# Performance work log

Measured on AMD Instinct MI355X. Metric: run time of the kernel, lower is better.

Reference implementation:

```python
import jax, jax.numpy as jnp
import numpy as np

TLAMBDA = 0.5
DELTA = 0.1
PROP_LAYERS = 2
LN_EPS = 1e-12
MASK_NEG = -10000.0
N_HEADS = 4


def _ln(x, g, b):
    m = x.mean(-1, keepdims=True)
    v = ((x - m) ** 2).mean(-1, keepdims=True)
    return (x - m) * jax.lax.rsqrt(v + LN_EPS) * g + b


def _l2norm(x):
    # F.normalize(p=2, dim=-1) with eps=1e-12
    n = jnp.sqrt((x * x).sum(-1, keepdims=True))
    return x / jnp.maximum(n, 1e-12)


def _sparse_prop(op):
    # op: [B, N, 2] rows of (col_idx, weight). result[b,j,m] = w_j*w_m if idx_j==idx_m else 0
    idx = op[..., 0].astype(jnp.int32)
    w = op[..., 1]
    eq = idx[:, :, None] == idx[:, None, :]
    return jnp.where(eq, w[:, :, None] * w[:, None, :], jnp.zeros((), op.dtype))


def _prop(t, P):
    enc = t
    for _ in range(PROP_LAYERS):
        t = jnp.einsum('bnm,bme->bne', P, t) + DELTA * enc
    return t


def _bert_layer(h, mask, Wq, bq, Wk, bk, Wv, bv, Wo, bo, g1, b1, Wi, bi, Wf, bf, g2, b2):
    AN, S, E = h.shape
    dh = E // N_HEADS

    def heads(x):
        return x.reshape(AN, S, N_HEADS, dh).transpose(0, 2, 1, 3)

    q = heads(h @ Wq + bq)
    k = heads(h @ Wk + bk)
    v = heads(h @ Wv + bv)
    scores = jnp.einsum('ahsd,ahtd->ahst', q, k) / np.float32(np.sqrt(dh)) + mask
    probs = jax.nn.softmax(scores, axis=-1)
    ctx = jnp.einsum('ahst,ahtd->ahsd', probs, v).transpose(0, 2, 1, 3).reshape(AN, S, E)
    a = _ln(ctx @ Wo + bo + h, g1, b1)
    f = jax.nn.gelu(a @ Wi + bi, approximate=False)
    return _ln(f @ Wf + bf + a, g2, b2)


def reference(token_edges_batch, hidden_states, attention_mask, query_embedding, key_embedding,
              user_operator, item_operator, distance_embedding, centrality_embedding,
              Wq, bq, Wk, bk, Wv, bv, Wo, bo, ln_att_g, ln_att_b, Wi, bi, Wf, bf, ln_ffn_g, ln_ffn_b,
              W_agg, b_agg, W_d1, b_d1, ln1_g, ln1_b, W_d2, b_d2, ln2_g, ln2_b):
    B, N, _ = token_edges_batch.shape
    AN, S, E = hidden_states.shape
    L = Wq.shape[0]

    U = _sparse_prop(user_operator)   # [B, N, N]
    I = _sparse_prop(item_operator)
    sub_next_q = jnp.zeros((B, N, E), hidden_states.dtype)
    sub_next_k = jnp.zeros((B, N, E), hidden_states.dtype)
    mask0 = attention_mask.at[..., :4].set(MASK_NEG)

    hs = hidden_states.reshape(B, N, S, E)
    all_hs = []
    for i in range(L):
        all_hs.append(hs)
        if i > 0:
            hs = (hs.at[:, :, 0].set(query_embedding)
                    .at[:, :, 1].set(key_embedding)
                    .at[:, :, 2].set(distance_embedding)
                    .at[:, :, 3].set(centrality_embedding))
        p1 = _ln(_prop(TLAMBDA * query_embedding + sub_next_q, U) @ W_d1 + b_d1, ln1_g, ln1_b)
        p2 = _ln(_prop(TLAMBDA * key_embedding + sub_next_k, I) @ W_d2 + b_d2, ln2_g, ln2_b)
        mask = mask0 if i == 0 else attention_mask
        h = _bert_layer(hs.reshape(AN, S, E), mask,
                        Wq[i], bq[i], Wk[i], bk[i], Wv[i], bv[i], Wo[i], bo[i],
                        ln_att_g[i], ln_att_b[i], Wi[i], bi[i], Wf[i], bf[i], ln_ffn_g[i], ln_ffn_b[i])
        hs = h.reshape(B, N, S, E)
        sub_next_q = hs[:, :, 0, :]
        sub_next_k = hs[:, :, 1, :]
        snt = _l2norm(hs[:, 0, 4, :])                       # [B, E]
        p = jnp.concatenate([snt, p1[:, 0, :], p2[:, 1, :]], axis=1)  # [B, 3E]
        agg = _l2norm(jax.nn.relu(p @ W_agg[i] + b_agg[i]))
        hs = hs.at[:, 0, 4, :].set(agg)
    all_hs.append(hs)

    out1 = all_hs[L - 1][:, 0, 4:, :].mean(axis=1)
    out2 = all_hs[L][:, 0, 4:, :].mean(axis=1)
    return 0.5 * (out1 + out2)


def setup_inputs() -> dict:
    key = jax.random.key(0)
    ks = jax.random.split(key, 40)
    B, N, S, E, L, FF = 64, 64, 32, 256, 2, 1024
    AN = B * N
    f = jnp.float32
    inp = {}
    inp['token_edges_batch'] = jax.random.randint(ks[0], (B, N, 8), 0, 100)
    inp['hidden_states'] = jax.random.normal(ks[1], (AN, S, E), f)
    inp['attention_mask'] = jnp.zeros((AN, 1, 1, S), f)
    inp['query_embedding'] = jax.random.normal(ks[2], (B, N, E), f)
    inp['key_embedding'] = jax.random.normal(ks[3], (B, N, E), f)
    inp['distance_embedding'] = jax.random.normal(ks[4], (B, N, E), f)
    inp['centrality_embedding'] = jax.random.normal(ks[5], (B, N, E), f)

    def make_op(k1, k2):
        idx = jax.random.randint(k1, (B, N), 0, 16).astype(f)
        w = jax.random.uniform(k2, (B, N), f)
        return jnp.stack([idx, w], axis=-1)

    inp['user_operator'] = make_op(ks[6], ks[7])
    inp['item_operator'] = make_op(ks[8], ks[9])

    sc = 0.02
    def w(k, shape):
        return jax.random.normal(k, shape, f) * sc

    inp['Wq'] = w(ks[10], (L, E, E)); inp['bq'] = jnp.zeros((L, E), f)
    inp['Wk'] = w(ks[11], (L, E, E)); inp['bk'] = jnp.zeros((L, E), f)
    inp['Wv'] = w(ks[12], (L, E, E)); inp['bv'] = jnp.zeros((L, E), f)
    inp['Wo'] = w(ks[13], (L, E, E)); inp['bo'] = jnp.zeros((L, E), f)
    inp['ln_att_g'] = jnp.ones((L, E), f); inp['ln_att_b'] = jnp.zeros((L, E), f)
    inp['Wi'] = w(ks[14], (L, E, FF)); inp['bi'] = jnp.zeros((L, FF), f)
    inp['Wf'] = w(ks[15], (L, FF, E)); inp['bf'] = jnp.zeros((L, E), f)
    inp['ln_ffn_g'] = jnp.ones((L, E), f); inp['ln_ffn_b'] = jnp.zeros((L, E), f)
    inp['W_agg'] = w(ks[16], (L, 3 * E, E)); inp['b_agg'] = jnp.zeros((L, E), f)
    inp['W_d1'] = w(ks[17], (E, E)); inp['b_d1'] = jnp.zeros((E,), f)
    inp['ln1_g'] = jnp.ones((E,), f); inp['ln1_b'] = jnp.zeros((E,), f)
    inp['W_d2'] = w(ks[18], (E, E)); inp['b_d2'] = jnp.zeros((E,), f)
    inp['ln2_g'] = jnp.ones((E,), f); inp['ln2_b'] = jnp.zeros((E,), f)
    return inp
```

## Files before the change

kernel.cpp:

```cpp
#include <hip/hip_runtime.h>
#include <math.h>

#define E 256
#define SEQ 32
#define FF 1024
#define NEG_MASK -10000.0f

typedef __attribute__((ext_vector_type(8))) short bf16x8;
typedef __attribute__((ext_vector_type(4))) short s16x4;
typedef __attribute__((ext_vector_type(4))) float f32x4;
typedef __attribute__((ext_vector_type(16))) float f32x16;

__device__ __forceinline__ float bf2f(unsigned short u) {
  unsigned v = ((unsigned)u) << 16; float f; __builtin_memcpy(&f, &v, 4); return f;
}
__device__ __forceinline__ unsigned short f2bf(float f) {
  unsigned u; __builtin_memcpy(&u, &f, 4);
  unsigned r = (u + 0x7fffu + ((u >> 16) & 1u)) >> 16;
  return (unsigned short)r;
}
__device__ __forceinline__ s16x4 f2bf4(float4 v) {
  s16x4 r;
  r[0] = (short)f2bf(v.x); r[1] = (short)f2bf(v.y);
  r[2] = (short)f2bf(v.z); r[3] = (short)f2bf(v.w);
  return r;
}
__device__ __forceinline__ f32x4 mfma16(bf16x8 a, bf16x8 b, f32x4 c) {
  return __builtin_amdgcn_mfma_f32_16x16x32_bf16(a, b, c, 0, 0, 0);
}
__device__ __forceinline__ f32x16 mfma32(bf16x8 a, bf16x8 b, f32x16 c) {
  return __builtin_amdgcn_mfma_f32_32x32x16_bf16(a, b, c, 0, 0, 0);
}
__device__ __forceinline__ float block_sum256(float v, float* tmp4) {
  #pragma unroll
  for (int o = 32; o > 0; o >>= 1) v += __shfl_down(v, o);
  int wid = threadIdx.x >> 6, lane = threadIdx.x & 63;
  if (lane == 0) tmp4[wid] = v;
  __syncthreads();
  float r = tmp4[0] + tmp4[1] + tmp4[2] + tmp4[3];
  __syncthreads();
  return r;
}

__global__ __launch_bounds__(256) void wprep_kernel(
    const float* __restrict__ Wq, const float* __restrict__ Wk,
    const float* __restrict__ Wv, const float* __restrict__ Wo,
    const float* __restrict__ Wi, const float* __restrict__ Wf,
    unsigned short* wqt, unsigned short* wkt, unsigned short* wvt,
    unsigned short* wot, unsigned short* wit, unsigned short* wft) {
  int type = blockIdx.y, ll = blockIdx.z, t = threadIdx.x;
  const float* src; unsigned short* dst; int Kd, Nd, m32;
  switch (type) {
    case 0: src = Wq + (size_t)ll * 65536;  dst = wqt + (size_t)ll * 65536;  Kd = 256;  Nd = 256;  m32 = 0; break;
    case 1: src = Wk + (size_t)ll * 65536;  dst = wkt + (size_t)ll * 65536;  Kd = 256;  Nd = 256;  m32 = 0; break;
    case 2: src = Wv + (size_t)ll * 65536;  dst = wvt + (size_t)ll * 65536;  Kd = 256;  Nd = 256;  m32 = 0; break;
    case 3: src = Wo + (size_t)ll * 65536;  dst = wot + (size_t)ll * 65536;  Kd = 256;  Nd = 256;  m32 = 0; break;
    case 4: src = Wi + (size_t)ll * 262144; dst = wit + (size_t)ll * 262144; Kd = 256;  Nd = 1024; m32 = 1; break;
    default: src = Wf + (size_t)ll * 262144; dst = wft + (size_t)ll * 262144; Kd = 1024; Nd = 256; m32 = 1; break;
  }
  int frag = blockIdx.x * 4 + (t >> 6);
  int l = t & 63;
  int nkc = m32 ? (Kd >> 4) : (Kd >> 5);
  int nfrag = (m32 ? (Nd >> 5) : (Nd >> 4)) * nkc;
  if (frag >= nfrag) return;
  int n, k0;
  if (m32) { n = (frag / nkc) * 32 + (l & 31); k0 = (frag % nkc) * 16 + (l >> 5) * 8; }
  else     { n = (frag / nkc) * 16 + (l & 15); k0 = (frag % nkc) * 32 + (l >> 4) * 8; }
  unsigned short vv[8];
  #pragma unroll
  for (int j = 0; j < 8; ++j) vv[j] = f2bf(src[(size_t)(k0 + j) * Nd + n]);
  unsigned short* o = dst + (size_t)frag * 512 + l * 8;
  #pragma unroll
  for (int j = 0; j < 8; ++j) o[j] = vv[j];
}

__global__ __launch_bounds__(256) void prop_ln_kernel(
    const float* __restrict__ emb_q, const float* __restrict__ emb_k,
    const float* snq,
    const float* __restrict__ uop, const float* __restrict__ iop,
    const float* __restrict__ Wd1, const float* __restrict__ bd1,
    const float* __restrict__ g1v, const float* __restrict__ b1v,
    const float* __restrict__ Wd2, const float* __restrict__ bd2,
    const float* __restrict__ g2v, const float* __restrict__ b2v,
    float* __restrict__ out1, float* __restrict__ out2) {
  int sel = blockIdx.y;
  const float* emb = sel ? emb_k : emb_q;
  const float* op  = sel ? iop : uop;
  const float* Wd  = sel ? Wd2 : Wd1;
  const float* bd  = sel ? bd2 : bd1;
  const float* g   = sel ? g2v : g1v;
  const float* bvec= sel ? b2v : b1v;
  float* outp      = sel ? out2 : out1;
  int row = sel;
  __shared__ float s1[16 * E];
  __shared__ float s2[16 * E];
  __shared__ float wv[64];
  __shared__ int gi[64];
  __shared__ float t2row[E];
  __shared__ float tmp4[4];
  int b = blockIdx.x, e = threadIdx.x;
  if (e < 64) {
    wv[e] = op[(b * 64 + e) * 2 + 1];
    gi[e] = (int)op[(b * 64 + e) * 2 + 0];
  }
  for (int gg = 0; gg < 16; ++gg) { s1[gg * E + e] = 0.f; s2[gg * E + e] = 0.f; }
  __syncthreads();
  float t0r = 0.f;
  for (int n = 0; n < 64; ++n) {
    float t0 = 0.5f * emb[(size_t)(b * 64 + n) * E + e];
    if (snq) t0 += snq[((size_t)(b * 64 + n) * 2 + sel) * E + e];
    if (n == row) t0r = t0;
    s1[gi[n] * E + e] += wv[n] * t0;
  }
  for (int n = 0; n < 64; ++n) {
    float t0 = 0.5f * emb[(size_t)(b * 64 + n) * E + e];
    if (snq) t0 += snq[((size_t)(b * 64 + n) * 2 + sel) * E + e];
    float t1 = wv[n] * s1[gi[n] * E + e] + 0.1f * t0;
    s2[gi[n] * E + e] += wv[n] * t1;
  }
  float t2 = wv[row] * s2[gi[row] * E + e] + 0.1f * t0r;
  t2row[e] = t2;
  __syncthreads();
  float y = bd[e];
  for (int k = 0; k < E; ++k) y = fmaf(t2row[k], Wd[k * E + e], y);
  float ssum = block_sum256(y, tmp4);
  float qsum = block_sum256(y * y, tmp4);
  float m = ssum * (1.f / E);
  float var = qsum * (1.f / E) - m * m;
  outp[b * E + e] = (y - m) * rsqrtf(var + 1e-12f) * g[e] + bvec[e];
}

__global__ __launch_bounds__(256, 4) void seq_attn_mfma(
    const float* __restrict__ hidden,
    const unsigned short* __restrict__ wqt, const float* __restrict__ bq,
    const unsigned short* __restrict__ wkt, const float* __restrict__ bk,
    const unsigned short* __restrict__ wvt, const float* __restrict__ bv,
    const float* __restrict__ mask, unsigned short* __restrict__ ctx_all,
    unsigned short* __restrict__ Kf, unsigned short* __restrict__ Vf) {
  __shared__ __align__(16) unsigned short aT[32][264];
  __shared__ __align__(16) unsigned short kvb[32][272];
  __shared__ __align__(16) unsigned short qs16[2][264];
  __shared__ float pr[4][2][36];
  int a = blockIdx.x, t = threadIdx.x;
  int w = t >> 6, l = t & 63;
  int lm = l & 15, lkq = l >> 4, lk = lkq << 3;
  size_t hb = (size_t)a * (SEQ * E);
  #pragma unroll
  for (int i = 0; i < 8; ++i) {
    int p = i * 256 + t; int row = p >> 6, c4 = (p & 63) << 2;
    float4 v = *(const float4*)&hidden[hb + row * E + c4];
    *(s16x4*)&aT[row][c4] = f2bf4(v);
  }
  __syncthreads();
  bool isn0 = ((a & 63) == 0);
  int nb = a >> 6;
  f32x4 zz = {0.f, 0.f, 0.f, 0.f};
  #pragma unroll
  for (int nt = 0; nt < 4; ++nt) {
    int ncol = w * 64 + nt * 16 + lm;
    const unsigned short* bkrow = wkt + ((size_t)(w * 4 + nt) * 8) * 512 + l * 8;
    const unsigned short* bqrow = wqt + ((size_t)(w * 4 + nt) * 8) * 512 + l * 8;
    bf16x8 bk8[8], bq8[8];
    #pragma unroll
    for (int kc = 0; kc < 8; ++kc) bk8[kc] = *(const bf16x8*)(bkrow + kc * 512);
    #pragma unroll
    for (int kc = 0; kc < 8; ++kc) bq8[kc] = *(const bf16x8*)(bqrow + kc * 512);
    f32x4 ak0 = zz, ak1 = zz, aq = zz;
    #pragma unroll
    for (int kc = 0; kc < 8; ++kc) {
      bf16x8 a0 = *(const bf16x8*)&aT[lm][kc * 32 + lk];
      bf16x8 a1 = *(const bf16x8*)&aT[16 + lm][kc * 32 + lk];
      ak0 = mfma16(a0, bk8[kc], ak0);
      ak1 = mfma16(a1, bk8[kc], ak1);
      aq  = mfma16(a0, bq8[kc], aq);
    }
    float bb = bk[ncol];
    #pragma unroll
    for (int r = 0; r < 4; ++r) {
      int rw = (lkq << 2) + r;
      float v0 = ak0[r] + bb, v1 = ak1[r] + bb;
      kvb[rw][ncol] = f2bf(v0);
      kvb[16 + rw][ncol] = f2bf(v1);
      if (isn0) {
        Kf[((size_t)nb * 32 + rw) * 256 + ncol] = f2bf(v0);
        Kf[((size_t)nb * 32 + 16 + rw) * 256 + ncol] = f2bf(v1);
      }
    }
    if (lkq == 0) {
      float bqv = bq[ncol];
      qs16[0][ncol] = f2bf(aq[0] + bqv);
      qs16[1][ncol] = f2bf(aq[1] + bqv);
    }
  }
  __syncthreads();
  {
    f32x4 sc0 = zz, sc1 = zz;
    #pragma unroll
    for (int kc2 = 0; kc2 < 2; ++kc2) {
      bf16x8 aq = *(const bf16x8*)&qs16[lm & 1][w * 64 + kc2 * 32 + lk];
      bf16x8 b0 = *(const bf16x8*)&kvb[lm][w * 64 + kc2 * 32 + lk];
      bf16x8 b1 = *(const bf16x8*)&kvb[16 + lm][w * 64 + kc2 * 32 + lk];
      sc0 = mfma16(aq, b0, sc0);
      sc1 = mfma16(aq, b1, sc1);
    }
    float mv0 = (lm < 4) ? NEG_MASK : mask[(size_t)a * SEQ + lm];
    float mv1 = mask[(size_t)a * SEQ + 16 + lm];
    #pragma unroll
    for (int r = 0; r < 2; ++r) {
      float s0 = sc0[r] * 0.125f + mv0;
      float s1 = sc1[r] * 0.125f + mv1;
      float mx = fmaxf(s0, s1);
      mx = fmaxf(mx, __shfl_xor(mx, 1));
      mx = fmaxf(mx, __shfl_xor(mx, 2));
      mx = fmaxf(mx, __shfl_xor(mx, 4));
      mx = fmaxf(mx, __shfl_xor(mx, 8));
      float e0 = expf(s0 - mx), e1 = expf(s1 - mx);
      float se = e0 + e1;
      se += __shfl_xor(se, 1); se += __shfl_xor(se, 2);
      se += __shfl_xor(se, 4); se += __shfl_xor(se, 8);
      float inv = 1.f / se;
      if (lkq == 0) {
        pr[w][r][lm] = e0 * inv;
        pr[w][r][16 + lm] = e1 * inv;
      }
    }
  }
  __syncthreads();
  #pragma unroll
  for (int nt = 0; nt < 4; ++nt) {
    int ncol = w * 64 + nt * 16 + lm;
    const unsigned short* bvrow = wvt + ((size_t)(w * 4 + nt) * 8) * 512 + l * 8;
    bf16x8 bv8[8];
    #pragma unroll
    for (int kc = 0; kc < 8; ++kc) bv8[kc] = *(const bf16x8*)(bvrow + kc * 512);
    f32x4 av0 = zz, av1 = zz;
    #pragma unroll
    for (int kc = 0; kc < 8; ++kc) {
      bf16x8 a0 = *(const bf16x8*)&aT[lm][kc * 32 + lk];
      bf16x8 a1 = *(const bf16x8*)&aT[16 + lm][kc * 32 + lk];
      av0 = mfma16(a0, bv8[kc], av0);
      av1 = mfma16(a1, bv8[kc], av1);
    }
    float bb = bv[ncol];
    #pragma unroll
    for (int r = 0; r < 4; ++r) {
      int rw = (lkq << 2) + r;
      float v0 = av0[r] + bb, v1 = av1[r] + bb;
      kvb[rw][ncol] = f2bf(v0);
      kvb[16 + rw][ncol] = f2bf(v1);
      if (isn0) {
        Vf[((size_t)nb * 32 + rw) * 256 + ncol] = f2bf(v0);
        Vf[((size_t)nb * 32 + 16 + rw) * 256 + ncol] = f2bf(v1);
      }
    }
  }
  __syncthreads();
  {
    float o0 = 0.f, o1 = 0.f;
    #pragma unroll
    for (int tt = 0; tt < 32; ++tt) {
      float vv = bf2f(kvb[tt][t]);
      o0 = fmaf(pr[w][0][tt], vv, o0);
      o1 = fmaf(pr[w][1][tt], vv, o1);
    }
    ctx_all[((size_t)a * 2 + 0) * E + t] = f2bf(o0);
    ctx_all[((size_t)a * 2 + 1) * E + t] = f2bf(o1);
  }
}

__global__ __launch_bounds__(256) void gemm_bias_kernel(
    const float* __restrict__ Af, const unsigned short* __restrict__ Bt,
    const float* __restrict__ bias, unsigned short* __restrict__ outb) {
  __shared__ __align__(16) unsigned short aT[32][264];
  int t = threadIdx.x, w = t >> 6, l = t & 63;
  int lm = l & 15, lkq = l >> 4, lk = lkq << 3;
  int row0 = blockIdx.x * 32;
  #pragma unroll
  for (int i = 0; i < 8; ++i) {
    int p = i * 256 + t; int row = p >> 6, c4 = (p & 63) << 2;
    int gr = row0 + row;
    int src = ((gr >> 5) << 11) + (gr & 31);
    float4 v = *(const float4*)&Af[(size_t)src * E + c4];
    *(s16x4*)&aT[row][c4] = f2bf4(v);
  }
  __syncthreads();
  f32x4 zz = {0.f, 0.f, 0.f, 0.f};
  #pragma unroll
  for (int nt = 0; nt < 4; ++nt) {
    int ncol = w * 64 + nt * 16 + lm;
    const unsigned short* brow = Bt + ((size_t)(w * 4 + nt) * 8) * 512 + l * 8;
    bf16x8 b8[8];
    #pragma unroll
    for (int kc = 0; kc < 8; ++kc) b8[kc] = *(const bf16x8*)(brow + kc * 512);
    f32x4 c0 = zz, c1 = zz;
    #pragma unroll
    for (int kc = 0; kc < 8; ++kc) {
      bf16x8 a0 = *(const bf16x8*)&aT[lm][kc * 32 + lk];
      bf16x8 a1 = *(const bf16x8*)&aT[16 + lm][kc * 32 + lk];
      c0 = mfma16(a0, b8[kc], c0);
      c1 = mfma16(a1, b8[kc], c1);
    }
    float bb = bias[ncol];
    #pragma unroll
    for (int r = 0; r < 4; ++r) {
      int rw = (lkq << 2) + r;
      outb[(size_t)(row0 + rw) * E + ncol] = f2bf(c0[r] + bb);
      outb[(size_t)(row0 + 16 + rw) * E + ncol] = f2bf(c1[r] + bb);
    }
  }
}

__global__ __launch_bounds__(256) void qkv1_kernel(
    const unsigned short* __restrict__ Ab,
    const unsigned short* __restrict__ wq, const float* __restrict__ bqv,
    const unsigned short* __restrict__ wk, const float* __restrict__ bkv,
    const unsigned short* __restrict__ wv, const float* __restrict__ bvv,
    unsigned short* q2, unsigned short* k2, unsigned short* v2) {
  __shared__ __align__(16) unsigned short aT[32][264];
  int t = threadIdx.x, w = t >> 6, l = t & 63;
  int lm = l & 15, lkq = l >> 4, lk = lkq << 3;
  int row0 = blockIdx.x * 32;
  int m = blockIdx.y;
  const unsigned short* Wt = (m == 0) ? wq : (m == 1) ? wk : wv;
  const float* bb = (m == 0) ? bqv : (m == 1) ? bkv : bvv;
  unsigned short* outb = (m == 0) ? q2 : (m == 1) ? k2 : v2;
  #pragma unroll
  for (int i = 0; i < 4; ++i) {
    int p = i * 256 + t; int row = p >> 5, c8 = (p & 31) << 3;
    *(s16x4*)&aT[row][c8] = *(const s16x4*)&Ab[(size_t)(row0 + row) * E + c8];
    *(s16x4*)&aT[row][c8 + 4] = *(const s16x4*)&Ab[(size_t)(row0 + row) * E + c8 + 4];
  }
  __syncthreads();
  f32x4 zz = {0.f, 0.f, 0.f, 0.f};
  #pragma unroll
  for (int nt = 0; nt < 4; ++nt) {
    int ncol = w * 64 + nt * 16 + lm;
    const unsigned short* brow = Wt + ((size_t)(w * 4 + nt) * 8) * 512 + l * 8;
    bf16x8 b8[8];
    #pragma unroll
    for (int kc = 0; kc < 8; ++kc) b8[kc] = *(const bf16x8*)(brow + kc * 512);
    f32x4 c0 = zz, c1 = zz;
    #pragma unroll
    for (int kc = 0; kc < 8; ++kc) {
      bf16x8 a0 = *(const bf16x8*)&aT[lm][kc * 32 + lk];
      bf16x8 a1 = *(const bf16x8*)&aT[16 + lm][kc * 32 + lk];
      c0 = mfma16(a0, b8[kc], c0);
      c1 = mfma16(a1, b8[kc], c1);
    }
    float bv2 = bb[ncol];
    #pragma unroll
    for (int r = 0; r < 4; ++r) {
      int rw = (lkq << 2) + r;
      outb[(size_t)(row0 + rw) * E + ncol] = f2bf(c0[r] + bv2);
      outb[(size_t)(row0 + 16 + rw) * E + ncol] = f2bf(c1[r] + bv2);
    }
  }
}

__global__ __launch_bounds__(256) void attnf_kernel(
    const unsigned short* __restrict__ Q, const unsigned short* __restrict__ K,
    const unsigned short* __restrict__ V, unsigned short* __restrict__ CTX,
    const float* __restrict__ mask, int set4) {
  int b = blockIdx.x, h = blockIdx.y, t = threadIdx.x;
  __shared__ float qsh[32][65], ksh[32][65], vsh[32][65];
  __shared__ float pr[32][33];
  size_t base = (size_t)b * (SEQ * E) + h * 64;
  for (int i = 0; i < 8; ++i) {
    int p = i * 256 + t; int s = p >> 6, d = p & 63;
    qsh[s][d] = bf2f(Q[base + s * E + d]);
    ksh[s][d] = bf2f(K[base + s * E + d]);
    vsh[s][d] = bf2f(V[base + s * E + d]);
  }
  __syncthreads();
  for (int i = 0; i < 4; ++i) {
    int p = i * 256 + t; int s = p >> 5, tt = p & 31;
    float acc = 0.f;
    #pragma unroll
    for (int d = 0; d < 64; ++d) acc = fmaf(qsh[s][d], ksh[tt][d], acc);
    float mv = mask[(size_t)b * 2048 + tt];
    if (set4 && tt < 4) mv = NEG_MASK;
    pr[s][tt] = acc * 0.125f + mv;
  }
  __syncthreads();
  int rrow = t >> 3, l8 = t & 7;
  float vals[4];
  float mx = -1e30f;
  #pragma unroll
  for (int ii = 0; ii < 4; ++ii) { vals[ii] = pr[rrow][l8 + ii * 8]; mx = fmaxf(mx, vals[ii]); }
  mx = fmaxf(mx, __shfl_xor(mx, 1));
  mx = fmaxf(mx, __shfl_xor(mx, 2));
  mx = fmaxf(mx, __shfl_xor(mx, 4));
  float se = 0.f;
  #pragma unroll
  for (int ii = 0; ii < 4; ++ii) { vals[ii] = expf(vals[ii] - mx); se += vals[ii]; }
  se += __shfl_xor(se, 1); se += __shfl_xor(se, 2); se += __shfl_xor(se, 4);
  float inv = 1.f / se;
  #pragma unroll
  for (int ii = 0; ii < 4; ++ii) pr[rrow][l8 + ii * 8] = vals[ii] * inv;
  __syncthreads();
  for (int i = 0; i < 8; ++i) {
    int p = i * 256 + t; int s = p >> 6, d = p & 63;
    float acc = 0.f;
    #pragma unroll
    for (int tt = 0; tt < SEQ; ++tt) acc = fmaf(pr[s][tt], vsh[tt][d], acc);
    CTX[base + s * E + d] = f2bf(acc);
  }
}

__device__ __forceinline__ int map_res(int gr) {
  if (gr < 8192) return ((gr >> 1) << 5) + (gr & 1);
  int rr = gr - 8192;
  return ((rr >> 5) << 11) + (rr & 31);
}

__global__ __launch_bounds__(256) void tailA_mfma(
    const unsigned short* __restrict__ ctx,
    const unsigned short* __restrict__ wo, const float* __restrict__ bo,
    const float* __restrict__ Res, int resmode,
    const float* __restrict__ g1, const float* __restrict__ b1,
    unsigned short* __restrict__ a_bf, float* __restrict__ a_f32) {
  __shared__ __align__(16) unsigned short aT[32][264];
  __shared__ float sT[32][257];
  __shared__ float prs[32][4], prq[32][4];
  int t = threadIdx.x, w = t >> 6, l = t & 63;
  int row0 = blockIdx.x * 32;
  #pragma unroll
  for (int i = 0; i < 8; ++i) {
    int p = i * 256 + t; int row = p >> 6, c4 = (p & 63) << 2;
    *(s16x4*)&aT[row][c4] = *(const s16x4*)&ctx[(size_t)(row0 + row) * E + c4];
  }
  __syncthreads();
  {
    int lm = l & 15, lkq = l >> 4, lk = lkq << 3;
    f32x4 zz = {0.f, 0.f, 0.f, 0.f};
    #pragma unroll
    for (int nt = 0; nt < 4; ++nt) {
      int ncol = w * 64 + nt * 16 + lm;
      const unsigned short* brow = wo + ((size_t)(w * 4 + nt) * 8) * 512 + l * 8;
      bf16x8 b8[8];
      #pragma unroll
      for (int kc = 0; kc < 8; ++kc) b8[kc] = *(const bf16x8*)(brow + kc * 512);
      f32x4 c0 = zz, c1 = zz;
      #pragma unroll
      for (int kc = 0; kc < 8; ++kc) {
        bf16x8 a0 = *(const bf16x8*)&aT[lm][kc * 32 + lk];
        bf16x8 a1 = *(const bf16x8*)&aT[16 + lm][kc * 32 + lk];
        c0 = mfma16(a0, b8[kc], c0);
        c1 = mfma16(a1, b8[kc], c1);
      }
      float bb = bo[ncol];
      #pragma unroll
      for (int r = 0; r < 4; ++r) {
        int rw = (lkq << 2) + r;
        int rr0 = resmode ? map_res(row0 + rw) : (row0 + rw);
        int rr1 = resmode ? map_res(row0 + 16 + rw) : (row0 + 16 + rw);
        sT[rw][ncol] = c0[r] + bb + Res[(size_t)rr0 * E + ncol];
        sT[16 + rw][ncol] = c1[r] + bb + Res[(size_t)rr1 * E + ncol];
      }
    }
  }
  __syncthreads();
  {
    int wid = t >> 6, lane = t & 63;
    float vcache[32];
    for (int r = 0; r < 32; ++r) {
      float v = sT[r][t];
      vcache[r] = v;
      float s = v, q = v * v;
      #pragma unroll
      for (int o = 32; o > 0; o >>= 1) { s += __shfl_down(s, o); q += __shfl_down(q, o); }
      if (lane == 0) { prs[r][wid] = s; prq[r][wid] = q; }
    }
    __syncthreads();
    #pragma unroll
    for (int r = 0; r < 32; ++r) {
      float Sv = prs[r][0] + prs[r][1] + prs[r][2] + prs[r][3];
      float Qv = prq[r][0] + prq[r][1] + prq[r][2] + prq[r][3];
      float m = Sv * (1.f / E), var = Qv * (1.f / E) - m * m;
      float val = (vcache[r] - m) * rsqrtf(var + 1e-12f) * g1[t] + b1[t];
      a_f32[(size_t)(row0 + r) * E + t] = val;
      a_bf[(size_t)(row0 + r) * E + t] = f2bf(val);
    }
  }
}

__global__ __launch_bounds__(512) void ffnB_kernel(
    const unsigned short* __restrict__ a_bf,
    const unsigned short* __restrict__ wi, const float* __restrict__ bi,
    const unsigned short* __restrict__ wf,
    unsigned short* __restrict__ part, size_t pstride) {
  __shared__ __align__(16) unsigned short aT[32][264];
  __shared__ __align__(16) unsigned short fT[32][264];
  int t = threadIdx.x, w = t >> 6, l = t & 63;
  int lm = l & 31, lk = (l >> 5) << 3;
  int row0 = blockIdx.x * 32, qh = blockIdx.y;
  #pragma unroll
  for (int i = 0; i < 2; ++i) {
    int chunk = i * 512 + t; int row = chunk >> 5, c8 = (chunk & 31) << 3;
    *(s16x4*)&aT[row][c8] = *(const s16x4*)&a_bf[(size_t)(row0 + row) * E + c8];
    *(s16x4*)&aT[row][c8 + 4] = *(const s16x4*)&a_bf[(size_t)(row0 + row) * E + c8 + 4];
  }
  __syncthreads();
  f32x16 zz16 = {0};
  {
    const unsigned short* brow = wi + ((size_t)(qh * 8 + w) * 16) * 512 + l * 8;
    bf16x8 b16[16];
    #pragma unroll
    for (int kc = 0; kc < 16; ++kc) b16[kc] = *(const bf16x8*)(brow + kc * 512);
    f32x16 c = zz16;
    #pragma unroll
    for (int kc = 0; kc < 16; ++kc) {
      bf16x8 a = *(const bf16x8*)&aT[lm][kc * 16 + lk];
      c = mfma32(a, b16[kc], c);
    }
    int lcol = w * 32 + lm;
    float bib = bi[qh * 256 + lcol];
    #pragma unroll
    for (int reg = 0; reg < 16; ++reg) {
      int row = (reg & 3) + 8 * (reg >> 2) + 4 * (l >> 5);
      float x = c[reg] + bib;
      fT[row][lcol] = f2bf(0.5f * x * (1.f + erff(x * 0.70710678118654752f)));
    }
  }
  __syncthreads();
  {
    const unsigned short* brow = wf + ((size_t)(w * 64 + qh * 16)) * 512 + l * 8;
    bf16x8 b16[16];
    #pragma unroll
    for (int kc = 0; kc < 16; ++kc) b16[kc] = *(const bf16x8*)(brow + kc * 512);
    f32x16 c = zz16;
    #pragma unroll
    for (int kc = 0; kc < 16; ++kc) {
      bf16x8 a = *(const bf16x8*)&fT[lm][kc * 16 + lk];
      c = mfma32(a, b16[kc], c);
    }
    unsigned short* po = part + (size_t)qh * pstride;
    int col = w * 32 + lm;
    #pragma unroll
    for (int reg = 0; reg < 16; ++reg) {
      int row = (reg & 3) + 8 * (reg >> 2) + 4 * (l >> 5);
      po[(size_t)(row0 + row) * E + col] = f2bf(c[reg]);
    }
  }
}

__global__ __launch_bounds__(256) void ffnC_kernel(
    const unsigned short* __restrict__ part, size_t pstride,
    const float* __restrict__ bfv, const float* __restrict__ a_f32,
    const float* __restrict__ g2, const float* __restrict__ b2,
    float* __restrict__ out0, float* __restrict__ out1, int split) {
  __shared__ float prs[32][4], prq[32][4];
  int t = threadIdx.x;
  int row0 = blockIdx.x * 32;
  int wid = t >> 6, lane = t & 63;
  float bb = bfv[t];
  float vcache[32];
  for (int r = 0; r < 32; ++r) {
    size_t idx = (size_t)(row0 + r) * E + t;
    float v = bf2f(part[idx]) + bf2f(part[pstride + idx]) +
              bf2f(part[2 * pstride + idx]) + bf2f(part[3 * pstride + idx]) +
              bb + a_f32[idx];
    vcache[r] = v;
    float s = v, q = v * v;
    #pragma unroll
    for (int o = 32; o > 0; o >>= 1) { s += __shfl_down(s, o); q += __shfl_down(q, o); }
    if (lane == 0) { prs[r][wid] = s; prq[r][wid] = q; }
  }
  __syncthreads();
  #pragma unroll
  for (int r = 0; r < 32; ++r) {
    float Sv = prs[r][0] + prs[r][1] + prs[r][2] + prs[r][3];
    float Qv = prq[r][0] + prq[r][1] + prq[r][2] + prq[r][3];
    float m = Sv * (1.f / E), var = Qv * (1.f / E) - m * m;
    float val = (vcache[r] - m) * rsqrtf(var + 1e-12f) * g2[t] + b2[t];
    int gr = row0 + r;
    if (gr < split) out0[(size_t)gr * E + t] = val;
    else            out1[(size_t)(gr - split) * E + t] = val;
  }
}

__global__ __launch_bounds__(256) void agg_build_kernel(
    const float* __restrict__ h1n0,
    const float* __restrict__ p1, const float* __restrict__ p2,
    const float* __restrict__ Wagg, const float* __restrict__ bagg,
    const float* __restrict__ qe, const float* __restrict__ ke,
    const float* __restrict__ de, const float* __restrict__ ce,
    float* __restrict__ agg0,
    float* __restrict__ h2f, unsigned short* __restrict__ h2b) {
  __shared__ float pv[768];
  __shared__ float tmp4[4];
  int b = blockIdx.x, t = threadIdx.x;
  float x = h1n0[(size_t)b * (SEQ * E) + 4 * E + t];
  float n2 = block_sum256(x * x, tmp4);
  pv[t] = x / fmaxf(sqrtf(n2), 1e-12f);
  pv[256 + t] = p1[b * E + t];
  pv[512 + t] = p2[b * E + t];
  __syncthreads();
  float y = bagg[t];
  for (int u = 0; u < 768; ++u) y = fmaf(pv[u], Wagg[u * E + t], y);
  y = fmaxf(y, 0.f);
  float n3 = block_sum256(y * y, tmp4);
  float aggv = y / fmaxf(sqrtf(n3), 1e-12f);
  agg0[b * E + t] = aggv;
  size_t eb = (size_t)(b * 64) * E + t;
  size_t ob = (size_t)b * (SEQ * E);
  float v;
  v = qe[eb];  h2f[ob + 0 * E + t] = v; h2b[ob + 0 * E + t] = f2bf(v);
  v = ke[eb];  h2f[ob + 1 * E + t] = v; h2b[ob + 1 * E + t] = f2bf(v);
  v = de[eb];  h2f[ob + 2 * E + t] = v; h2b[ob + 2 * E + t] = f2bf(v);
  v = ce[eb];  h2f[ob + 3 * E + t] = v; h2b[ob + 3 * E + t] = f2bf(v);
  h2f[ob + 4 * E + t] = aggv; h2b[ob + 4 * E + t] = f2bf(aggv);
  for (int s = 5; s < SEQ; ++s) {
    v = h1n0[ob + s * E + t];
    h2f[ob + s * E + t] = v; h2b[ob + s * E + t] = f2bf(v);
  }
}

__global__ __launch_bounds__(256) void agg_out_kernel(
    const float* __restrict__ h2,
    const float* __restrict__ p1, const float* __restrict__ p2,
    const float* __restrict__ Wagg, const float* __restrict__ bagg,
    const float* __restrict__ h1n0, const float* __restrict__ agg0,
    float* __restrict__ outp) {
  __shared__ float pv[768];
  __shared__ float tmp4[4];
  int b = blockIdx.x, t = threadIdx.x;
  float x = h2[(size_t)b * (SEQ * E) + 4 * E + t];
  float n2 = block_sum256(x * x, tmp4);
  pv[t] = x / fmaxf(sqrtf(n2), 1e-12f);
  pv[256 + t] = p1[b * E + t];
  pv[512 + t] = p2[b * E + t];
  __syncthreads();
  float y = bagg[t];
  for (int u = 0; u < 768; ++u) y = fmaf(pv[u], Wagg[u * E + t], y);
  y = fmaxf(y, 0.f);
  float n3 = block_sum256(y * y, tmp4);
  float agg1v = y / fmaxf(sqrtf(n3), 1e-12f);
  size_t ob = (size_t)b * (SEQ * E);
  float s1v = agg0[b * E + t];
  float s2v = agg1v;
  for (int s = 5; s < SEQ; ++s) { s1v += h1n0[ob + s * E + t]; s2v += h2[ob + s * E + t]; }
  outp[b * E + t] = 0.5f * (s1v + s2v) * (1.f / 28.f);
}

extern "C" void kernel_launch(void* const* d_in, const int* in_sizes, int n_in,
                              void* d_out, int out_size, void* d_ws, size_t ws_size,
                              hipStream_t stream) {
  (void)in_sizes; (void)n_in; (void)out_size;
  const float* hidden = (const float*)d_in[1];
  const float* amask  = (const float*)d_in[2];
  const float* qemb   = (const float*)d_in[3];
  const float* kemb   = (const float*)d_in[4];
  const float* demb   = (const float*)d_in[5];
  const float* cemb   = (const float*)d_in[6];
  const float* uop    = (const float*)d_in[7];
  const float* iop    = (const float*)d_in[8];
  const float* Wq = (const float*)d_in[9];  const float* bq = (const float*)d_in[10];
  const float* Wk = (const float*)d_in[11]; const float* bk = (const float*)d_in[12];
  const float* Wv = (const float*)d_in[13]; const float* bv = (const float*)d_in[14];
  const float* Wo = (const float*)d_in[15]; const float* bo = (const float*)d_in[16];
  const float* g1 = (const float*)d_in[17]; const float* b1 = (const float*)d_in[18];
  const float* Wi = (const float*)d_in[19]; const float* bi = (const float*)d_in[20];
  const float* Wf = (const float*)d_in[21]; const float* bf = (const float*)d_in[22];
  const float* g2 = (const float*)d_in[23]; const float* b2 = (const float*)d_in[24];
  const float* Wagg = (const float*)d_in[25]; const float* bagg = (const float*)d_in[26];
  const float* Wd1 = (const float*)d_in[27]; const float* bd1 = (const float*)d_in[28];
  const float* l1g = (const float*)d_in[29]; const float* l1b = (const float*)d_in[30];
  const float* Wd2 = (const float*)d_in[31]; const float* bd2 = (const float*)d_in[32];
  const float* l2g = (const float*)d_in[33]; const float* l2b = (const float*)d_in[34];

  char* cur = (char*)d_ws;
  auto alloc_us = [&](size_t n) { unsigned short* p = (unsigned short*)cur; cur += ((n * 2 + 255) & ~(size_t)255); return p; };
  auto alloc_f  = [&](size_t n) { float* p = (float*)cur; cur += ((n * 4 + 255) & ~(size_t)255); return p; };
  unsigned short* wqt = alloc_us(131072);
  unsigned short* wkt = alloc_us(131072);
  unsigned short* wvt = alloc_us(131072);
  unsigned short* wot = alloc_us(131072);
  unsigned short* wit = alloc_us(524288);
  unsigned short* wft = alloc_us(524288);
  unsigned short* ctx_all = alloc_us((size_t)10240 * 256);
  unsigned short* qn0 = alloc_us((size_t)2048 * 256);
  unsigned short* Kf  = alloc_us((size_t)2048 * 256);
  unsigned short* Vf  = alloc_us((size_t)2048 * 256);
  unsigned short* h2inb = alloc_us((size_t)2048 * 256);
  unsigned short* a_bf = alloc_us((size_t)10240 * 256);
  unsigned short* q2b = alloc_us((size_t)2048 * 256);
  unsigned short* k2b = alloc_us((size_t)2048 * 256);
  unsigned short* v2b = alloc_us((size_t)2048 * 256);
  unsigned short* ctx1 = alloc_us((size_t)2048 * 256);
  unsigned short* part = alloc_us((size_t)4 * 10240 * 256);
  float* a_f32 = alloc_f((size_t)10240 * 256);
  float* h101  = alloc_f((size_t)4096 * 2 * 256);
  float* h1n0  = alloc_f((size_t)2048 * 256);
  float* h2inf = alloc_f((size_t)2048 * 256);
  float* h2    = alloc_f((size_t)2048 * 256);
  float* p1_0  = alloc_f(64 * 256);
  float* p2_0  = alloc_f(64 * 256);
  float* p1_1  = alloc_f(64 * 256);
  float* p2_1  = alloc_f(64 * 256);
  float* agg0  = alloc_f(64 * 256);
  if ((size_t)(cur - (char*)d_ws) > ws_size) return;
  const size_t PSTRIDE = (size_t)10240 * 256;

  wprep_kernel<<<dim3(128, 6, 2), 256, 0, stream>>>(Wq, Wk, Wv, Wo, Wi, Wf,
                                                    wqt, wkt, wvt, wot, wit, wft);

  prop_ln_kernel<<<dim3(64, 2), 256, 0, stream>>>(qemb, kemb, nullptr, uop, iop,
                                                  Wd1, bd1, l1g, l1b, Wd2, bd2, l2g, l2b,
                                                  p1_0, p2_0);
  seq_attn_mfma<<<4096, 256, 0, stream>>>(hidden, wqt, bq, wkt, bk, wvt, bv,
                                          amask, ctx_all, Kf, Vf);
  gemm_bias_kernel<<<64, 256, 0, stream>>>(hidden, wqt, bq, qn0);
  attnf_kernel<<<dim3(64, 4), 256, 0, stream>>>(qn0, Kf, Vf, ctx_all + (size_t)8192 * 256,
                                                amask, 1);
  tailA_mfma<<<320, 256, 0, stream>>>(ctx_all, wot, bo, hidden, 1, g1, b1, a_bf, a_f32);
  ffnB_kernel<<<dim3(320, 4), 512, 0, stream>>>(a_bf, wit, bi, wft, part, PSTRIDE);
  ffnC_kernel<<<320, 256, 0, stream>>>(part, PSTRIDE, bf, a_f32, g2, b2,
                                       h101, h1n0, 8192);
  agg_build_kernel<<<64, 256, 0, stream>>>(h1n0, p1_0, p2_0, Wagg, bagg,
                                           qemb, kemb, demb, cemb, agg0, h2inf, h2inb);

  prop_ln_kernel<<<dim3(64, 2), 256, 0, stream>>>(qemb, kemb, h101, uop, iop,
                                                  Wd1, bd1, l1g, l1b, Wd2, bd2, l2g, l2b,
                                                  p1_1, p2_1);
  qkv1_kernel<<<dim3(64, 3), 256, 0, stream>>>(h2inb,
                                               wqt + 65536, bq + E,
                                               wkt + 65536, bk + E,
                                               wvt + 65536, bv + E,
                                               q2b, k2b, v2b);
  attnf_kernel<<<dim3(64, 4), 256, 0, stream>>>(q2b, k2b, v2b, ctx1, amask, 0);
  tailA_mfma<<<64, 256, 0, stream>>>(ctx1, wot + 65536, bo + E, h2inf, 0,
                                     g1 + E, b1 + E, a_bf, a_f32);
  ffnB_kernel<<<dim3(64, 4), 512, 0, stream>>>(a_bf, wit + 262144, bi + FF,
                                               wft + 262144, part, PSTRIDE);
  ffnC_kernel<<<64, 256, 0, stream>>>(part, PSTRIDE, bf + E, a_f32,
                                      g2 + E, b2 + E, h2, h2, 1 << 30);
  agg_out_kernel<<<64, 256, 0, stream>>>(h2, p1_1, p2_1,
                                         Wagg + (size_t)768 * E, bagg + E,
                                         h1n0, agg0, (float*)d_out);
}
```

Measured before the change: 382.8 us.

## Fuse attention output projection and LayerNorm into FFN up-projection kernel

```diff
diff --git a/kernel.cpp b/kernel.cpp
--- a/kernel.cpp
+++ b/kernel.cpp
@@ -413,20 +413,24 @@
   return ((rr >> 5) << 11) + (rr & 31);
 }
 
-__global__ __launch_bounds__(256) void tailA_mfma(
+__global__ __launch_bounds__(512) void ffnB_kernel(
     const unsigned short* __restrict__ ctx,
     const unsigned short* __restrict__ wo, const float* __restrict__ bo,
     const float* __restrict__ Res, int resmode,
     const float* __restrict__ g1, const float* __restrict__ b1,
-    unsigned short* __restrict__ a_bf, float* __restrict__ a_f32) {
-  __shared__ __align__(16) unsigned short aT[32][264];
-  __shared__ float sT[32][257];
+    const unsigned short* __restrict__ wi, const float* __restrict__ bi,
+    const unsigned short* __restrict__ wf,
+    float* __restrict__ a_f32, unsigned short* __restrict__ part, size_t pstride) {
+  __shared__ __align__(16) char smem[16896 + 32896];
+  unsigned short (*aT)[264] = (unsigned short(*)[264])smem;
+  float (*sT)[257] = (float(*)[257])(smem + 16896);
+  unsigned short (*fT)[264] = (unsigned short(*)[264])(smem + 16896);
   __shared__ float prs[32][4], prq[32][4];
   int t = threadIdx.x, w = t >> 6, l = t & 63;
-  int row0 = blockIdx.x * 32;
-  #pragma unroll
-  for (int i = 0; i < 8; ++i) {
-    int p = i * 256 + t; int row = p >> 6, c4 = (p & 63) << 2;
+  int row0 = blockIdx.x * 32, qh = blockIdx.y;
+  #pragma unroll
+  for (int i = 0; i < 4; ++i) {
+    int p = i * 512 + t; int row = p >> 6, c4 = (p & 63) << 2;
     *(s16x4*)&aT[row][c4] = *(const s16x4*)&ctx[(size_t)(row0 + row) * E + c4];
   }
   __syncthreads();
@@ -434,9 +438,9 @@
     int lm = l & 15, lkq = l >> 4, lk = lkq << 3;
     f32x4 zz = {0.f, 0.f, 0.f, 0.f};
     #pragma unroll
-    for (int nt = 0; nt < 4; ++nt) {
-      int ncol = w * 64 + nt * 16 + lm;
-      const unsigned short* brow = wo + ((size_t)(w * 4 + nt) * 8) * 512 + l * 8;
+    for (int nt = 0; nt < 2; ++nt) {
+      int ncol = w * 32 + nt * 16 + lm;
+      const unsigned short* brow = wo + ((size_t)(w * 2 + nt) * 8) * 512 + l * 8;
       bf16x8 b8[8];
       #pragma unroll
       for (int kc = 0; kc < 8; ++kc) b8[kc] = *(const bf16x8*)(brow + kc * 512);
@@ -463,44 +467,31 @@
   {
     int wid = t >> 6, lane = t & 63;
     float vcache[32];
-    for (int r = 0; r < 32; ++r) {
-      float v = sT[r][t];
-      vcache[r] = v;
-      float s = v, q = v * v;
+    if (t < 256) {
+      for (int r = 0; r < 32; ++r) {
+        float v = sT[r][t];
+        vcache[r] = v;
+        float s = v, q = v * v;
+        #pragma unroll
+        for (int o = 32; o > 0; o >>= 1) { s += __shfl_down(s, o); q += __shfl_down(q, o); }
+        if (lane == 0) { prs[r][wid] = s; prq[r][wid] = q; }
+      }
+    }
+    __syncthreads();
+    if (t < 256) {
       #pragma unroll
-      for (int o = 32; o > 0; o >>= 1) { s += __shfl_down(s, o); q += __shfl_down(q, o); }
-      if (lane == 0) { prs[r][wid] = s; prq[r][wid] = q; }
+      for (int r = 0; r < 32; ++r) {
+        float Sv = prs[r][0] + prs[r][1] + prs[r][2] + prs[r][3];
+        float Qv = prq[r][0] + prq[r][1] + prq[r][2] + prq[r][3];
+        float m = Sv * (1.f / E), var = Qv * (1.f / E) - m * m;
+        float val = (vcache[r] - m) * rsqrtf(var + 1e-12f) * g1[t] + b1[t];
+        aT[r][t] = f2bf(val);
+        if (qh == 0) a_f32[(size_t)(row0 + r) * E + t] = val;
+      }
     }
     __syncthreads();
-    #pragma unroll
-    for (int r = 0; r < 32; ++r) {
-      float Sv = prs[r][0] + prs[r][1] + prs[r][2] + prs[r][3];
-      float Qv = prq[r][0] + prq[r][1] + prq[r][2] + prq[r][3];
-      float m = Sv * (1.f / E), var = Qv * (1.f / E) - m * m;
-      float val = (vcache[r] - m) * rsqrtf(var + 1e-12f) * g1[t] + b1[t];
-      a_f32[(size_t)(row0 + r) * E + t] = val;
-      a_bf[(size_t)(row0 + r) * E + t] = f2bf(val);
-    }
-  }
-}
-
-__global__ __launch_bounds__(512) void ffnB_kernel(
-    const unsigned short* __restrict__ a_bf,
-    const unsigned short* __restrict__ wi, const float* __restrict__ bi,
-    const unsigned short* __restrict__ wf,
-    unsigned short* __restrict__ part, size_t pstride) {
-  __shared__ __align__(16) unsigned short aT[32][264];
-  __shared__ __align__(16) unsigned short fT[32][264];
-  int t = threadIdx.x, w = t >> 6, l = t & 63;
+  }
   int lm = l & 31, lk = (l >> 5) << 3;
-  int row0 = blockIdx.x * 32, qh = blockIdx.y;
-  #pragma unroll
-  for (int i = 0; i < 2; ++i) {
-    int chunk = i * 512 + t; int row = chunk >> 5, c8 = (chunk & 31) << 3;
-    *(s16x4*)&aT[row][c8] = *(const s16x4*)&a_bf[(size_t)(row0 + row) * E + c8];
-    *(s16x4*)&aT[row][c8 + 4] = *(const s16x4*)&a_bf[(size_t)(row0 + row) * E + c8 + 4];
-  }
-  __syncthreads();
   f32x16 zz16 = {0};
   {
     const unsigned short* brow = wi + ((size_t)(qh * 8 + w) * 16) * 512 + l * 8;
@@ -683,7 +674,6 @@
   unsigned short* Kf  = alloc_us((size_t)2048 * 256);
   unsigned short* Vf  = alloc_us((size_t)2048 * 256);
   unsigned short* h2inb = alloc_us((size_t)2048 * 256);
-  unsigned short* a_bf = alloc_us((size_t)10240 * 256);
   unsigned short* q2b = alloc_us((size_t)2048 * 256);
   unsigned short* k2b = alloc_us((size_t)2048 * 256);
   unsigned short* v2b = alloc_us((size_t)2048 * 256);
@@ -713,8 +703,8 @@
   gemm_bias_kernel<<<64, 256, 0, stream>>>(hidden, wqt, bq, qn0);
   attnf_kernel<<<dim3(64, 4), 256, 0, stream>>>(qn0, Kf, Vf, ctx_all + (size_t)8192 * 256,
                                                 amask, 1);
-  tailA_mfma<<<320, 256, 0, stream>>>(ctx_all, wot, bo, hidden, 1, g1, b1, a_bf, a_f32);
-  ffnB_kernel<<<dim3(320, 4), 512, 0, stream>>>(a_bf, wit, bi, wft, part, PSTRIDE);
+  ffnB_kernel<<<dim3(320, 4), 512, 0, stream>>>(ctx_all, wot, bo, hidden, 1, g1, b1,
+                                                wit, bi, wft, a_f32, part, PSTRIDE);
   ffnC_kernel<<<320, 256, 0, stream>>>(part, PSTRIDE, bf, a_f32, g2, b2,
                                        h101, h1n0, 8192);
   agg_build_kernel<<<64, 256, 0, stream>>>(h1n0, p1_0, p2_0, Wagg, bagg,
@@ -729,10 +719,10 @@
                                                wvt + 65536, bv + E,
                                                q2b, k2b, v2b);
   attnf_kernel<<<dim3(64, 4), 256, 0, stream>>>(q2b, k2b, v2b, ctx1, amask, 0);
-  tailA_mfma<<<64, 256, 0, stream>>>(ctx1, wot + 65536, bo + E, h2inf, 0,
-                                     g1 + E, b1 + E, a_bf, a_f32);
-  ffnB_kernel<<<dim3(64, 4), 512, 0, stream>>>(a_bf, wit + 262144, bi + FF,
-                                               wft + 262144, part, PSTRIDE);
+  ffnB_kernel<<<dim3(64, 4), 512, 0, stream>>>(ctx1, wot + 65536, bo + E, h2inf, 0,
+                                               g1 + E, b1 + E,
+                                               wit + 262144, bi + FF, wft + 262144,
+                                               a_f32, part, PSTRIDE);
   ffnC_kernel<<<64, 256, 0, stream>>>(part, PSTRIDE, bf + E, a_f32,
                                       g2 + E, b2 + E, h2, h2, 1 << 30);
   agg_out_kernel<<<64, 256, 0, stream>>>(h2, p1_1, p2_1,
```

After: 398.9 us. 1.04x slower.
